# Performance work log

Hardware: AMD Instinct MI355X
Metric: run time of the kernel (lower is better)

The kernel has to match this reference:

```python
import jax, jax.numpy as jnp
import numpy as np

N = 65536      # flattened tokens
K = 8192       # codebook_size
D = 64         # codebook_dim
DECAY = 0.9
EPS = 1e-05


def setup_inputs() -> dict:
    key = jax.random.key(0)
    k1, k2, k3, k4 = jax.random.split(key, 4)
    z = jax.random.normal(k1, (N, D), dtype=jnp.float32)
    # codebook initialized uniform(-1, 1) in the torch module
    weight = jax.random.uniform(k2, (K, D), dtype=jnp.float32, minval=-1.0, maxval=1.0)
    # EMA state: positive cluster sizes, embed_avg near the codebook
    cluster_size = jax.random.uniform(k3, (K,), dtype=jnp.float32)
    embed_avg = weight + 0.01 * jax.random.normal(k4, (K, D), dtype=jnp.float32)
    return {"z": z, "weight": weight, "cluster_size": cluster_size, "embed_avg": embed_avg}


def reference(z, weight, cluster_size, embed_avg):
    # VectorQuantizer.ema_update: distances -> argmin -> gather -> EMA stats -> weight refresh
    zd = jax.lax.stop_gradient(z)  # torch uses z.detach() for distance/quant_error
    # distance[n,k] = ||z_n||^2 + ||c_k||^2 - 2 z_n . c_k   (addmm pattern)
    dist = (zd * zd).sum(1, keepdims=True) + (weight * weight).sum(1) - 2.0 * (zd @ weight.T)  # [N, K]
    token = jnp.argmin(dist, axis=1)                      # [N]
    embed = weight[token]                                  # gather [N, D]
    quant_error = jnp.mean(((embed - zd) ** 2).sum(1))

    # onehot_probs.sum(0) == per-code counts; onehot.T @ z == segment sum of z
    counts = jax.ops.segment_sum(jnp.ones((zd.shape[0],), zd.dtype), token, num_segments=K)  # [K]
    embed_sum = jax.ops.segment_sum(z, token, num_segments=K)                                # [K, D]

    new_cluster_size = cluster_size * DECAY + (1.0 - DECAY) * counts
    new_embed_avg = embed_avg * DECAY + (1.0 - DECAY) * embed_sum

    # ema_weight_update with num_tokens = codebook_size
    n = new_cluster_size.sum()
    smoothed = (new_cluster_size + EPS) / (n + K * EPS) * n
    new_weight = new_embed_avg / smoothed[:, None]

    return quant_error, new_weight, new_cluster_size, new_embed_avg
```

## Files before the change

kernel.cpp:

```cpp
#include <hip/hip_runtime.h>
#include <type_traits>

#define N_TOK 65536
#define K_CODE 8192
#define D_DIM 64

constexpr float DECAY = 0.9f;
constexpr float OMD = 0.1f;
constexpr float EPS = 1e-5f;

constexpr int OUT_QE = 0;
constexpr int OUT_W  = 1;
constexpr int OUT_CS = 1 + K_CODE * D_DIM;
constexpr int OUT_EA = OUT_CS + K_CODE;

constexpr int WS_QE     = 0;
constexpr int WS_NSUM   = 16;
constexpr int WS_COUNTS = 16 + 8 * 32;
constexpr int WS_EMBSUM = WS_COUNTS + K_CODE;
constexpr int WS_WHI    = WS_EMBSUM + K_CODE * D_DIM;
constexpr int WS_WLO    = WS_WHI + K_CODE * D_DIM / 2;
constexpr int WS_CNF    = WS_WLO + K_CODE * D_DIM / 2;
constexpr int WS_ZERO   = WS_WHI;

typedef __attribute__((ext_vector_type(16))) float floatx16;
typedef __attribute__((ext_vector_type(8)))  short short8;
typedef __attribute__((ext_vector_type(8)))  __bf16 bf16x8;

template <typename T, typename = void> struct mfma_takes : std::false_type {};
template <typename T>
struct mfma_takes<T, std::void_t<decltype(__builtin_amdgcn_mfma_f32_32x32x16_bf16(
    std::declval<T>(), std::declval<T>(), std::declval<floatx16>(), 0, 0, 0))>>
    : std::true_type {};

__device__ __forceinline__ floatx16 MFMA(short8 a, short8 b, floatx16 c) {
  if constexpr (mfma_takes<bf16x8>::value) {
    return __builtin_amdgcn_mfma_f32_32x32x16_bf16(
        __builtin_bit_cast(bf16x8, a), __builtin_bit_cast(bf16x8, b), c, 0, 0, 0);
  } else {
    return __builtin_amdgcn_mfma_f32_32x32x16_bf16(a, b, c, 0, 0, 0);
  }
}

__device__ __forceinline__ unsigned short bf16rne(float x) {
  unsigned int u = __float_as_uint(x);
  return (unsigned short)((u + 0x7FFFu + ((u >> 16) & 1u)) >> 16);
}

__device__ __forceinline__ void gload_lds16(const unsigned short* g, unsigned short* l) {
#if defined(__has_builtin) && __has_builtin(__builtin_amdgcn_global_load_lds)
  typedef __attribute__((address_space(1))) void gvoid;
  typedef __attribute__((address_space(3))) void lvoid;
  __builtin_amdgcn_global_load_lds((gvoid*)g, (lvoid*)l, 16, 0, 0);
#else
  *(uint4*)l = *(const uint4*)g;
#endif
}

__global__ void vq_prep(const float* __restrict__ w, const float* __restrict__ cs,
                        float* __restrict__ ws) {
  const int tid = threadIdx.x;
  const int d = tid & 63;
  const int kw = tid >> 6;
  const int k = blockIdx.x * 4 + kw;
  const float v = w[(size_t)k * D_DIM + d];
  const unsigned short h = bf16rne(v);
  const float hf = __uint_as_float((unsigned int)h << 16);
  const unsigned short l = bf16rne(v - hf);
  unsigned short* whi = (unsigned short*)(ws + WS_WHI);
  unsigned short* wlo = (unsigned short*)(ws + WS_WLO);
  const int pos = k * D_DIM + (((d >> 3) ^ (k & 7)) * 8) + (d & 7);
  whi[pos] = h;
  wlo[pos] = l;
  float s = v * v;
#pragma unroll
  for (int m = 32; m >= 1; m >>= 1) s += __shfl_xor(s, m);
  __shared__ float csp[4];
  if (d == 0) {
    (ws + WS_CNF)[k] = s + 64.0f;
    csp[kw] = cs[k];
  }
  __syncthreads();
  if (tid == 0) {
    atomicAdd(ws + WS_NSUM + ((blockIdx.x & 7) << 5),
              DECAY * (csp[0] + csp[1] + csp[2] + csp[3]));
  }
}

__global__ __launch_bounds__(512, 4) void vq_argmin(
    const float* __restrict__ z, float* __restrict__ ws)
{
  __shared__ __align__(16) unsigned short Wbuf[2][4][2][32 * 64];
  __shared__ float mind_s[2][128];
  __shared__ int   tok_s[2][128];

  const int tid  = threadIdx.x;
  const int w    = tid >> 6;
  const int lane = tid & 63;
  const int m    = lane & 31;
  const int h    = lane >> 5;
  const int tg   = w & 3;
  const int hw   = w >> 2;
  const int tb   = blockIdx.x * 128;

  const unsigned short* whi = (const unsigned short*)(ws + WS_WHI);
  const unsigned short* wlo = (const unsigned short*)(ws + WS_WLO);
  const float*          cnf = ws + WS_CNF;

  short8 ah[4], al[4];
  float znorm = 0.f;
  {
    const float* zrow = z + (size_t)(tb + tg * 32 + m) * D_DIM + 8 * h;
#pragma unroll
    for (int s4 = 0; s4 < 4; ++s4) {
      const float4 v0 = *(const float4*)(zrow + 16 * s4);
      const float4 v1 = *(const float4*)(zrow + 16 * s4 + 4);
      const float vals[8] = {v0.x, v0.y, v0.z, v0.w, v1.x, v1.y, v1.z, v1.w};
#pragma unroll
      for (int j = 0; j < 8; ++j) {
        const float x = vals[j];
        znorm += x * x;
        const float y = -2.0f * x;
        const unsigned short hb = bf16rne(y);
        const float hf = __uint_as_float((unsigned int)hb << 16);
        const unsigned short lb = bf16rne(y - hf);
        ah[s4][j] = (short)hb;
        al[s4][j] = (short)lb;
      }
    }
    znorm += __shfl_xor(znorm, 32);
  }

  float kmin[16];
#pragma unroll
  for (int r = 0; r < 16; ++r) kmin[r] = 3.4e38f;

  auto issueStage = [&](int sIdx, int bufIdx) {
#pragma unroll
    for (int i = 0; i < 2; ++i) {
      const int t = w * 2 + i;
      const int half = t >> 3, plane = (t >> 2) & 1, seg = t & 3;
      const unsigned short* src = (plane ? wlo : whi)
          + ((size_t)half * 4096 + (size_t)sIdx * 32) * D_DIM + seg * 512 + lane * 8;
      unsigned short* dst = &Wbuf[half][bufIdx][plane][seg * 512];
      gload_lds16(src, dst);
    }
  };

  int xoff[4];
#pragma unroll
  for (int s4 = 0; s4 < 4; ++s4) xoff[s4] = ((2 * s4 + h) ^ (m & 7)) * 8;
  const int mrow = m * 64;
  const int cbase = hw * 4096;

#define LOADBH(BH, BUF) do {                                          \
    const unsigned short* _p = &Wbuf[hw][(BUF)][0][mrow];             \
    BH[0] = *(const short8*)(_p + xoff[0]);                           \
    BH[1] = *(const short8*)(_p + xoff[1]);                           \
    BH[2] = *(const short8*)(_p + xoff[2]);                           \
    BH[3] = *(const short8*)(_p + xoff[3]);                           \
  } while (0)

#define LOADBL(BL, BUF) do {                                          \
    const unsigned short* _p = &Wbuf[hw][(BUF)][1][mrow];             \
    BL[0] = *(const short8*)(_p + xoff[0]);                           \
    BL[1] = *(const short8*)(_p + xoff[1]);                           \
    BL[2] = *(const short8*)(_p + xoff[2]);                           \
    BL[3] = *(const short8*)(_p + xoff[3]);                           \
  } while (0)

  issueStage(0, 0);
  issueStage(1, 1);
  float cn_cur = cnf[cbase + m];
  asm volatile("s_waitcnt vmcnt(0)" ::: "memory");
  __builtin_amdgcn_s_barrier();
  asm volatile("" ::: "memory");

  short8 bh[4], bl[4];
  LOADBH(bh, 0);

  for (int s = 0; s < 128; ++s) {
    issueStage((s + 2) & 127, (s + 2) & 3);
    const float cn_next = cnf[cbase + ((s + 1) & 127) * 32 + m];
    asm volatile("s_waitcnt vmcnt(3)" ::: "memory");
    __builtin_amdgcn_s_barrier();
    asm volatile("" ::: "memory");

    LOADBL(bl, s & 3);

    floatx16 acc;
#pragma unroll
    for (int r = 0; r < 16; ++r) acc[r] = cn_cur;

    __builtin_amdgcn_s_setprio(1);
    acc = MFMA(ah[0], bh[0], acc); acc = MFMA(ah[1], bh[1], acc);
    acc = MFMA(ah[2], bh[2], acc); acc = MFMA(ah[3], bh[3], acc);
    acc = MFMA(al[0], bh[0], acc); acc = MFMA(al[1], bh[1], acc);
    acc = MFMA(al[2], bh[2], acc); acc = MFMA(al[3], bh[3], acc);
    __builtin_amdgcn_s_setprio(0);

    LOADBH(bh, (s + 1) & 3);
    __builtin_amdgcn_s_setprio(1);
    acc = MFMA(ah[0], bl[0], acc); acc = MFMA(ah[1], bl[1], acc);
    acc = MFMA(ah[2], bl[2], acc); acc = MFMA(ah[3], bl[3], acc);
    __builtin_amdgcn_s_setprio(0);

#pragma unroll
    for (int r = 0; r < 16; ++r) {
      kmin[r] = fminf(kmin[r],
          __uint_as_float((__float_as_uint(acc[r]) & 0xFFFFFF00u) | (unsigned)s));
    }
    cn_cur = cn_next;
  }
#undef LOADBH
#undef LOADBL

#pragma unroll
  for (int r = 0; r < 16; ++r) {
    float kv = kmin[r];
    int mo = m;
#pragma unroll
    for (int mm = 1; mm < 32; mm <<= 1) {
      const float ov = __shfl_xor(kv, mm);
      const int   om = __shfl_xor(mo, mm);
      if (ov < kv || (ov == kv && om < mo)) { kv = ov; mo = om; }
    }
    const int mr = (r & 3) + 8 * (r >> 2) + 4 * h;
    if (m == mr) {
      const unsigned int kb = __float_as_uint(kv);
      tok_s[hw][tg * 32 + mr] = hw * 4096 + (int)(kb & 0xFFu) * 32 + mo;
      mind_s[hw][tg * 32 + mr] =
          __uint_as_float(kb & 0xFFFFFF00u) - 64.0f + znorm;
    }
  }
  __syncthreads();

  float* counts = ws + WS_COUNTS;
  float* embsum = ws + WS_EMBSUM;

  if (tid < 128) {
    const float d0 = mind_s[0][tid], d1 = mind_s[1][tid];
    const int   i0 = tok_s[0][tid],  i1 = tok_s[1][tid];
    const bool t1 = d1 < d0;
    const float dm = t1 ? d1 : d0;
    const int   im = t1 ? i1 : i0;
    tok_s[0][tid] = im;
    float qe = dm;
#pragma unroll
    for (int mm = 32; mm >= 1; mm >>= 1) qe += __shfl_xor(qe, mm);
    if ((tid & 63) == 0) atomicAdd(ws + WS_QE, qe);
    atomicAdd(&counts[im], 1.0f);
  }
  __syncthreads();

#pragma unroll 4
  for (int t = 0; t < 16; ++t) {
    const int row = w * 16 + t;
    const int tk = tok_s[0][row];
    const float zv = z[(size_t)(tb + row) * D_DIM + lane];
    atomicAdd(&embsum[(size_t)tk * D_DIM + lane], zv);
  }
}

__global__ void vq_finalize(const float* __restrict__ cluster_size,
                            const float* __restrict__ embed_avg,
                            const float* __restrict__ ws, float* __restrict__ out)
{
  const int idx = blockIdx.x * 256 + threadIdx.x;
  const int k = idx >> 6;
  const float ncs = cluster_size[k] * DECAY + OMD * ws[WS_COUNTS + k];
  const float nea = embed_avg[idx] * DECAY + OMD * ws[WS_EMBSUM + idx];
  out[OUT_EA + idx] = nea;
  float n = OMD * (float)N_TOK;
#pragma unroll
  for (int i = 0; i < 8; ++i) n += ws[WS_NSUM + (i << 5)];
  const float sm = (ncs + EPS) / (n + K_CODE * EPS) * n;
  out[OUT_W + idx] = nea / sm;
  if ((idx & 63) == 0) out[OUT_CS + k] = ncs;
  if (idx == 0) out[OUT_QE] = ws[WS_QE] * (1.0f / N_TOK);
}

extern "C" void kernel_launch(void* const* d_in, const int* in_sizes, int n_in,
                              void* d_out, int out_size, void* d_ws, size_t ws_size,
                              hipStream_t stream) {
  const float* z  = (const float*)d_in[0];
  const float* w  = (const float*)d_in[1];
  const float* cs = (const float*)d_in[2];
  const float* ea = (const float*)d_in[3];
  float* out = (float*)d_out;
  float* ws  = (float*)d_ws;

  (void)hipMemsetAsync(d_ws, 0, (size_t)WS_ZERO * sizeof(float), stream);

  vq_prep<<<K_CODE / 4, 256, 0, stream>>>(w, cs, ws);
  vq_argmin<<<N_TOK / 128, 512, 0, stream>>>(z, ws);
  vq_finalize<<<K_CODE * D_DIM / 256, 256, 0, stream>>>(cs, ea, ws, out);
}
```

Measured before the change: 271.3 us.

## Double token tile per block to reuse codebook fragments across two MFMA streams

Each wave now holds two 32-token A fragments and runs two interleaved accumulator chains against the same staged codebook fragments. This halves codebook LDS traffic and global staging per token and gives the MFMA pipe two independent dependency chains. The cost is more registers, so launch bounds drop to 2 blocks per CU and the grid halves. Separately, zeroing of counts and embsum moves from the memset into vq_prep, leaving a much smaller memset.

```diff
diff --git a/kernel.cpp b/kernel.cpp
--- a/kernel.cpp
+++ b/kernel.cpp
@@ -21,7 +21,6 @@
 constexpr int WS_WHI    = WS_EMBSUM + K_CODE * D_DIM;
 constexpr int WS_WLO    = WS_WHI + K_CODE * D_DIM / 2;
 constexpr int WS_CNF    = WS_WLO + K_CODE * D_DIM / 2;
-constexpr int WS_ZERO   = WS_WHI;
 
 typedef __attribute__((ext_vector_type(16))) float floatx16;
 typedef __attribute__((ext_vector_type(8)))  short short8;
@@ -60,6 +59,10 @@
 __global__ void vq_prep(const float* __restrict__ w, const float* __restrict__ cs,
                         float* __restrict__ ws) {
   const int tid = threadIdx.x;
+  const int gid = blockIdx.x * 256 + tid;
+  ws[WS_EMBSUM + gid] = 0.0f;
+  if (gid < K_CODE) ws[WS_COUNTS + gid] = 0.0f;
+
   const int d = tid & 63;
   const int kw = tid >> 6;
   const int k = blockIdx.x * 4 + kw;
@@ -87,30 +90,31 @@
   }
 }
 
-__global__ __launch_bounds__(512, 4) void vq_argmin(
+__global__ __launch_bounds__(512, 2) void vq_argmin(
     const float* __restrict__ z, float* __restrict__ ws)
 {
   __shared__ __align__(16) unsigned short Wbuf[2][4][2][32 * 64];
-  __shared__ float mind_s[2][128];
-  __shared__ int   tok_s[2][128];
+  __shared__ float mind_s[2][256];
+  __shared__ int   tok_s[2][256];
 
   const int tid  = threadIdx.x;
   const int w    = tid >> 6;
   const int lane = tid & 63;
   const int m    = lane & 31;
   const int h    = lane >> 5;
-  const int tg   = w & 3;
+  const int tgp  = w & 3;
   const int hw   = w >> 2;
-  const int tb   = blockIdx.x * 128;
+  const int tb   = blockIdx.x * 256;
 
   const unsigned short* whi = (const unsigned short*)(ws + WS_WHI);
   const unsigned short* wlo = (const unsigned short*)(ws + WS_WLO);
   const float*          cnf = ws + WS_CNF;
 
-  short8 ah[4], al[4];
-  float znorm = 0.f;
-  {
-    const float* zrow = z + (size_t)(tb + tg * 32 + m) * D_DIM + 8 * h;
+  short8 ah_a[4], al_a[4], ah_b[4], al_b[4];
+  float znorm_a = 0.f, znorm_b = 0.f;
+  auto loadA = [&](int sub, short8* AH, short8* AL, float& zn) {
+    const float* zrow =
+        z + (size_t)(tb + tgp * 64 + sub * 32 + m) * D_DIM + 8 * h;
 #pragma unroll
     for (int s4 = 0; s4 < 4; ++s4) {
       const float4 v0 = *(const float4*)(zrow + 16 * s4);
@@ -119,21 +123,23 @@
 #pragma unroll
       for (int j = 0; j < 8; ++j) {
         const float x = vals[j];
-        znorm += x * x;
+        zn += x * x;
         const float y = -2.0f * x;
         const unsigned short hb = bf16rne(y);
         const float hf = __uint_as_float((unsigned int)hb << 16);
         const unsigned short lb = bf16rne(y - hf);
-        ah[s4][j] = (short)hb;
-        al[s4][j] = (short)lb;
+        AH[s4][j] = (short)hb;
+        AL[s4][j] = (short)lb;
       }
     }
-    znorm += __shfl_xor(znorm, 32);
-  }
-
-  float kmin[16];
-#pragma unroll
-  for (int r = 0; r < 16; ++r) kmin[r] = 3.4e38f;
+    zn += __shfl_xor(zn, 32);
+  };
+  loadA(0, ah_a, al_a, znorm_a);
+  loadA(1, ah_b, al_b, znorm_b);
+
+  float kmin0[16], kmin1[16];
+#pragma unroll
+  for (int r = 0; r < 16; ++r) { kmin0[r] = 3.4e38f; kmin1[r] = 3.4e38f; }
 
   auto issueStage = [&](int sIdx, int bufIdx) {
 #pragma unroll
@@ -188,57 +194,71 @@
 
     LOADBL(bl, s & 3);
 
-    floatx16 acc;
-#pragma unroll
-    for (int r = 0; r < 16; ++r) acc[r] = cn_cur;
+    floatx16 acc0, acc1;
+#pragma unroll
+    for (int r = 0; r < 16; ++r) { acc0[r] = cn_cur; acc1[r] = cn_cur; }
 
     __builtin_amdgcn_s_setprio(1);
-    acc = MFMA(ah[0], bh[0], acc); acc = MFMA(ah[1], bh[1], acc);
-    acc = MFMA(ah[2], bh[2], acc); acc = MFMA(ah[3], bh[3], acc);
-    acc = MFMA(al[0], bh[0], acc); acc = MFMA(al[1], bh[1], acc);
-    acc = MFMA(al[2], bh[2], acc); acc = MFMA(al[3], bh[3], acc);
+    acc0 = MFMA(ah_a[0], bh[0], acc0); acc1 = MFMA(ah_b[0], bh[0], acc1);
+    acc0 = MFMA(ah_a[1], bh[1], acc0); acc1 = MFMA(ah_b[1], bh[1], acc1);
+    acc0 = MFMA(ah_a[2], bh[2], acc0); acc1 = MFMA(ah_b[2], bh[2], acc1);
+    acc0 = MFMA(ah_a[3], bh[3], acc0); acc1 = MFMA(ah_b[3], bh[3], acc1);
+    acc0 = MFMA(al_a[0], bh[0], acc0); acc1 = MFMA(al_b[0], bh[0], acc1);
+    acc0 = MFMA(al_a[1], bh[1], acc0); acc1 = MFMA(al_b[1], bh[1], acc1);
+    acc0 = MFMA(al_a[2], bh[2], acc0); acc1 = MFMA(al_b[2], bh[2], acc1);
+    acc0 = MFMA(al_a[3], bh[3], acc0); acc1 = MFMA(al_b[3], bh[3], acc1);
     __builtin_amdgcn_s_setprio(0);
 
     LOADBH(bh, (s + 1) & 3);
     __builtin_amdgcn_s_setprio(1);
-    acc = MFMA(ah[0], bl[0], acc); acc = MFMA(ah[1], bl[1], acc);
-    acc = MFMA(ah[2], bl[2], acc); acc = MFMA(ah[3], bl[3], acc);
+    acc0 = MFMA(ah_a[0], bl[0], acc0); acc1 = MFMA(ah_b[0], bl[0], acc1);
+    acc0 = MFMA(ah_a[1], bl[1], acc0); acc1 = MFMA(ah_b[1], bl[1], acc1);
+    acc0 = MFMA(ah_a[2], bl[2], acc0); acc1 = MFMA(ah_b[2], bl[2], acc1);
+    acc0 = MFMA(ah_a[3], bl[3], acc0); acc1 = MFMA(ah_b[3], bl[3], acc1);
     __builtin_amdgcn_s_setprio(0);
 
 #pragma unroll
     for (int r = 0; r < 16; ++r) {
-      kmin[r] = fminf(kmin[r],
-          __uint_as_float((__float_as_uint(acc[r]) & 0xFFFFFF00u) | (unsigned)s));
+      kmin0[r] = fminf(kmin0[r],
+          __uint_as_float((__float_as_uint(acc0[r]) & 0xFFFFFF00u) | (unsigned)s));
+      kmin1[r] = fminf(kmin1[r],
+          __uint_as_float((__float_as_uint(acc1[r]) & 0xFFFFFF00u) | (unsigned)s));
     }
     cn_cur = cn_next;
   }
 #undef LOADBH
 #undef LOADBL
 
-#pragma unroll
-  for (int r = 0; r < 16; ++r) {
-    float kv = kmin[r];
-    int mo = m;
-#pragma unroll
-    for (int mm = 1; mm < 32; mm <<= 1) {
-      const float ov = __shfl_xor(kv, mm);
-      const int   om = __shfl_xor(mo, mm);
-      if (ov < kv || (ov == kv && om < mo)) { kv = ov; mo = om; }
-    }
-    const int mr = (r & 3) + 8 * (r >> 2) + 4 * h;
-    if (m == mr) {
-      const unsigned int kb = __float_as_uint(kv);
-      tok_s[hw][tg * 32 + mr] = hw * 4096 + (int)(kb & 0xFFu) * 32 + mo;
-      mind_s[hw][tg * 32 + mr] =
-          __uint_as_float(kb & 0xFFFFFF00u) - 64.0f + znorm;
-    }
-  }
+#define REDUCE_WRITE(KM, SUB, ZN) do {                                      \
+    _Pragma("unroll")                                                       \
+    for (int r = 0; r < 16; ++r) {                                          \
+      float kv = KM[r];                                                     \
+      int mo = m;                                                           \
+      _Pragma("unroll")                                                     \
+      for (int mm = 1; mm < 32; mm <<= 1) {                                 \
+        const float ov = __shfl_xor(kv, mm);                                \
+        const int   om = __shfl_xor(mo, mm);                                \
+        if (ov < kv || (ov == kv && om < mo)) { kv = ov; mo = om; }         \
+      }                                                                     \
+      const int mr = (r & 3) + 8 * (r >> 2) + 4 * h;                        \
+      if (m == mr) {                                                        \
+        const unsigned int kb = __float_as_uint(kv);                        \
+        const int trow = tgp * 64 + (SUB) * 32 + mr;                        \
+        tok_s[hw][trow] = hw * 4096 + (int)(kb & 0xFFu) * 32 + mo;          \
+        mind_s[hw][trow] = __uint_as_float(kb & 0xFFFFFF00u) - 64.0f + (ZN);\
+      }                                                                     \
+    }                                                                       \
+  } while (0)
+
+  REDUCE_WRITE(kmin0, 0, znorm_a);
+  REDUCE_WRITE(kmin1, 1, znorm_b);
+#undef REDUCE_WRITE
   __syncthreads();
 
   float* counts = ws + WS_COUNTS;
   float* embsum = ws + WS_EMBSUM;
 
-  if (tid < 128) {
+  if (tid < 256) {
     const float d0 = mind_s[0][tid], d1 = mind_s[1][tid];
     const int   i0 = tok_s[0][tid],  i1 = tok_s[1][tid];
     const bool t1 = d1 < d0;
@@ -254,8 +274,8 @@
   __syncthreads();
 
 #pragma unroll 4
-  for (int t = 0; t < 16; ++t) {
-    const int row = w * 16 + t;
+  for (int t = 0; t < 32; ++t) {
+    const int row = w * 32 + t;
     const int tk = tok_s[0][row];
     const float zv = z[(size_t)(tb + row) * D_DIM + lane];
     atomicAdd(&embsum[(size_t)tk * D_DIM + lane], zv);
@@ -290,9 +310,9 @@
   float* out = (float*)d_out;
   float* ws  = (float*)d_ws;
 
-  (void)hipMemsetAsync(d_ws, 0, (size_t)WS_ZERO * sizeof(float), stream);
+  (void)hipMemsetAsync(d_ws, 0, (size_t)WS_COUNTS * sizeof(float), stream);
 
   vq_prep<<<K_CODE / 4, 256, 0, stream>>>(w, cs, ws);
-  vq_argmin<<<N_TOK / 128, 512, 0, stream>>>(z, ws);
+  vq_argmin<<<N_TOK / 256, 512, 0, stream>>>(z, ws);
   vq_finalize<<<K_CODE * D_DIM / 256, 256, 0, stream>>>(cs, ea, ws, out);
 }
```

Result: slower. 279.0 us (+2.8%).
